# Performance work log

Hardware: AMD Instinct MI355X
Metric: run time of the kernel (lower is better)

Reference implementation:

```python
import jax, jax.numpy as jnp
import numpy as np

EPS = 1e-5


def _ln(t):
    # Custom LayerNorm from the source: unbiased variance (torch.var default),
    # gamma=ones, beta=zeros (plain tensors, never trained) -> plain normalize.
    m = t.mean(axis=-1, keepdims=True)
    v = t.var(axis=-1, keepdims=True, ddof=1)
    return (t - m) / jnp.sqrt(v + EPS)


def setup_inputs() -> dict:
    key = jax.random.key(0)
    B, T, C, H = 4, 2048, 1024, 16
    hs = C // H
    ks = jax.random.split(key, 10)
    s_in = (1.0 / C) ** 0.5   # nn.Linear default init scale (approx, uniform->normal ok for ref)
    s_ff = (1.0 / (4 * C)) ** 0.5
    return {
        "x": jax.random.normal(ks[0], (B, T, C), jnp.float32),
        "Wq": jax.random.normal(ks[1], (H, C, hs), jnp.float32) * s_in,
        "Wk": jax.random.normal(ks[2], (H, C, hs), jnp.float32) * s_in,
        "Wv": jax.random.normal(ks[3], (H, C, hs), jnp.float32) * s_in,
        "Wo": jax.random.normal(ks[4], (C, C), jnp.float32) * s_in,
        "bo": jnp.zeros((C,), jnp.float32),
        "W1": jax.random.normal(ks[5], (C, 4 * C), jnp.float32) * s_in,
        "b1": jnp.zeros((4 * C,), jnp.float32),
        "W2": jax.random.normal(ks[6], (4 * C, C), jnp.float32) * s_ff,
        "b2": jnp.zeros((C,), jnp.float32),
    }


def reference(x, Wq, Wk, Wv, Wo, bo, W1, b1, W2, b2):
    B, T, C = x.shape
    H, _, hs = Wq.shape
    # per-head projections (equivalent to the Python loop over Head modules)
    q = jnp.einsum('btc,hcd->bhtd', x, Wq)
    k = jnp.einsum('btc,hcd->bhtd', x, Wk)
    v = jnp.einsum('btc,hcd->bhtd', x, Wv)
    scores = jnp.einsum('bhtd,bhsd->bhts', q, k) * (hs ** -0.5)
    causal = jnp.tril(jnp.ones((T, T), dtype=bool))
    scores = jnp.where(causal, scores, jnp.float32(-jnp.inf))
    w = jax.nn.softmax(scores, axis=-1)          # dropout is identity in eval
    o = jnp.einsum('bhts,bhsd->bhtd', w, v)
    o = o.transpose(0, 2, 1, 3).reshape(B, T, C)  # concat heads
    attn = o @ Wo + bo
    x1 = x + _ln(attn)
    ff = jax.nn.relu(x1 @ W1 + b1) @ W2 + b2
    return x1 + _ln(ff)
```

## Files before the change

kernel.cpp:

```cpp
#include <hip/hip_runtime.h>
#include <hip/hip_bf16.h>

using bf16 = __hip_bfloat16;
typedef __attribute__((ext_vector_type(8))) short s8v;
typedef __attribute__((ext_vector_type(4))) float f4v;
typedef __attribute__((ext_vector_type(16))) float f16v;
typedef __attribute__((ext_vector_type(4))) unsigned int u4v;

#define QSCALE 0.18033688011112042f

__device__ __forceinline__ void gld_lds16(const void* g, void* l) {
  __builtin_amdgcn_global_load_lds(
      (const __attribute__((address_space(1))) void*)g,
      (__attribute__((address_space(3))) void*)l, 16, 0, 0);
}

__device__ __forceinline__ unsigned short bfbits(float f) {
  bf16 t = __float2bfloat16(f);
  return *reinterpret_cast<unsigned short*>(&t);
}

__device__ __forceinline__ unsigned int pk2(float lo, float hi) {
  return (unsigned int)bfbits(lo) | ((unsigned int)bfbits(hi) << 16);
}

__device__ __forceinline__ void lswap(unsigned int& a, unsigned int& b) {
  asm("v_permlane32_swap_b32 %0, %1" : "+v"(a), "+v"(b));
}

__global__ __launch_bounds__(256) void f32_to_bf16_k(const float* __restrict__ in,
                                                     bf16* __restrict__ out, size_t n) {
  const size_t i = ((size_t)blockIdx.x * 256 + threadIdx.x) * 4;
  if (i + 3 < n) {
    const float4 v = *(const float4*)(in + i);
    out[i + 0] = __float2bfloat16(v.x);
    out[i + 1] = __float2bfloat16(v.y);
    out[i + 2] = __float2bfloat16(v.z);
    out[i + 3] = __float2bfloat16(v.w);
  }
}

__global__ __launch_bounds__(256) void tr_to_bf16_k(const float* __restrict__ in,
                                                    bf16* __restrict__ out,
                                                    int R, int C,
                                                    size_t inb, size_t outb) {
  __shared__ float tile[32][33];
  in  += (size_t)blockIdx.z * inb;
  out += (size_t)blockIdx.z * outb;
  const int r0 = blockIdx.y * 32, c0 = blockIdx.x * 32;
  const int tx = threadIdx.x & 31, ty = threadIdx.x >> 5;
#pragma unroll
  for (int i = 0; i < 4; ++i)
    tile[ty + i * 8][tx] = in[(size_t)(r0 + ty + i * 8) * C + c0 + tx];
  __syncthreads();
#pragma unroll
  for (int i = 0; i < 4; ++i)
    out[(size_t)(c0 + ty + i * 8) * R + r0 + tx] = __float2bfloat16(tile[tx][ty + i * 8]);
}

template <int MODE, int BN>
__global__ __launch_bounds__(512, 2) void gemmT(const bf16* __restrict__ A,
                                                const bf16* __restrict__ B,
                                                const float* __restrict__ bias,
                                                float* __restrict__ Cf,
                                                bf16* __restrict__ Cb,
                                                bf16* __restrict__ Vout,
                                                int M, int N, int K) {
  constexpr int NF = BN / 64;
  constexpr int BH = BN / 128;
  __shared__ __attribute__((aligned(16))) bf16 AS[2][256 * 64];
  __shared__ __attribute__((aligned(16))) bf16 BS[2][BN * 64];

  const int tid  = threadIdx.x;
  const int wid  = tid >> 6;
  const int lane = tid & 63;
  const int l16  = lane & 15;
  const int quad = lane >> 4;
  const int wm   = wid >> 2;
  const int wn   = wid & 3;

  const int gx  = gridDim.x;
  const int nwg = gx * gridDim.y;
  int lin = blockIdx.y * gx + blockIdx.x;
  lin = (lin & 7) * (nwg >> 3) + (lin >> 3);
  const int bm = (lin / gx) * 256;
  const int bn = (lin % gx) * BN;

  const int d0 = tid * 16;
  const int a0 = d0 ^ (((d0 >> 9) & 1) << 5);
  const int sr = a0 >> 7;
  const int scol = (a0 & 127) >> 1;
  const bf16* Asrc = A + (size_t)(bm + sr) * K + scol;
  const bf16* Bsrc = B + (size_t)(bn + sr) * K + scol;
  char* const AW0 = (char*)&AS[0][0] + wid * 1024;
  char* const AW1 = (char*)&AS[1][0] + wid * 1024;
  char* const BW0 = (char*)&BS[0][0] + wid * 1024;
  char* const BW1 = (char*)&BS[1][0] + wid * 1024;

  const int sq16 = (quad * 16) ^ (((l16 >> 2) & 1) << 5);
  const int rdA  = l16 * 128 + sq16;
  const int rdB  = wn * (BN / 4) * 128 + l16 * 128 + sq16;

#define STAGE_A2(dst, src) \
  do { gld_lds16((src), (dst)); gld_lds16((src) + (size_t)64 * K, (dst) + 8192); } while (0)
#define STAGE_BH(dst, src) \
  do { gld_lds16((src), (dst)); \
       if constexpr (BH == 2) gld_lds16((src) + (size_t)64 * K, (dst) + 8192); } while (0)
#define WAIT_B_INFLIGHT() \
  do { if constexpr (BN == 256) asm volatile("s_waitcnt vmcnt(4)" ::: "memory"); \
       else                     asm volatile("s_waitcnt vmcnt(2)" ::: "memory"); } while (0)

  f4v acc[8][NF];
#pragma unroll
  for (int i = 0; i < 8; ++i)
#pragma unroll
    for (int j = 0; j < NF; ++j) acc[i][j] = (f4v){0.f, 0.f, 0.f, 0.f};

  const int NT = K >> 6;

  STAGE_A2(AW0,         Asrc);
  STAGE_A2(AW0 + 16384, Asrc + (size_t)128 * K);
  STAGE_BH(BW0,             Bsrc);
  STAGE_BH(BW0 + BH * 8192, Bsrc + (size_t)(BH * 64) * K);
  STAGE_BH(BW1,             Bsrc + 64);
  STAGE_BH(BW1 + BH * 8192, Bsrc + (size_t)(BH * 64) * K + 64);
  WAIT_B_INFLIGHT();
  asm volatile("s_barrier" ::: "memory");

  s8v bfrag[NF][2];
  for (int u = 0; u < NT; ++u) {
    const int bsel = u & 1;
    const char* Ard = (char*)&AS[bsel][0] + wm * 16384 + rdA;
    const char* Brd = (char*)&BS[bsel][0] + rdB;
    char* const AWn = bsel ? AW0 : AW1;
    char* const BWc = bsel ? BW1 : BW0;
    const bf16* An = Asrc + (size_t)(u + 1) * 64;
    const bf16* Bn = Bsrc + (size_t)(u + 2) * 64;
#pragma unroll
    for (int p = 0; p < 4; ++p) {
      s8v afrag[2][2];
#pragma unroll
      for (int j = 0; j < 2; ++j)
#pragma unroll
        for (int kk = 0; kk < 2; ++kk)
          afrag[j][kk] = *(const s8v*)(Ard + (p * 2 + j) * 2048 + kk * 64);
      if (p == 0) {
#pragma unroll
        for (int nf = 0; nf < NF; ++nf)
#pragma unroll
          for (int kk = 0; kk < 2; ++kk)
            bfrag[nf][kk] = *(const s8v*)(Brd + nf * 2048 + kk * 64);
      }
      if (p == 0 && u + 1 < NT) STAGE_A2(AWn,         An);
      if (p == 1 && u + 1 < NT) STAGE_A2(AWn + 16384, An + (size_t)128 * K);
      if (p == 2 && u + 2 < NT) STAGE_BH(BWc,             Bn);
      if (p == 3 && u + 2 < NT) STAGE_BH(BWc + BH * 8192, Bn + (size_t)(BH * 64) * K);
      asm volatile("s_barrier" ::: "memory");
      asm volatile("s_waitcnt lgkmcnt(0)" ::: "memory");
      __builtin_amdgcn_sched_barrier(0);
      __builtin_amdgcn_s_setprio(1);
#pragma unroll
      for (int kk = 0; kk < 2; ++kk)
#pragma unroll
        for (int j = 0; j < 2; ++j)
#pragma unroll
          for (int nf = 0; nf < NF; ++nf)
            acc[p * 2 + j][nf] = __builtin_amdgcn_mfma_f32_16x16x32_bf16(
                afrag[j][kk], bfrag[nf][kk], acc[p * 2 + j][nf], 0, 0, 0);
      __builtin_amdgcn_s_setprio(0);
      if (p == 3) {
        if (u + 2 < NT) WAIT_B_INFLIGHT();
        else            asm volatile("s_waitcnt vmcnt(0)" ::: "memory");
      }
      asm volatile("s_barrier" ::: "memory");
    }
  }
#undef STAGE_A2
#undef STAGE_BH
#undef WAIT_B_INFLIGHT

  const size_t ldc = (size_t)N;
#pragma unroll
  for (int mf = 0; mf < 8; ++mf) {
#pragma unroll
    for (int nf = 0; nf < NF; ++nf) {
      const int col  = bn + wn * (BN / 4) + nf * 16 + l16;
      const int row0 = bm + wm * 128 + mf * 16 + quad * 4;
      if (MODE == 0) {
        if (col < 2048) {
          const float sc = (col < 1024) ? QSCALE : 1.0f;
#pragma unroll
          for (int r = 0; r < 4; ++r)
            Cb[(size_t)(row0 + r) * ldc + col] = __float2bfloat16(acc[mf][nf][r] * sc);
        } else {
          ushort4 pk;
          pk.x = bfbits(acc[mf][nf][0]);
          pk.y = bfbits(acc[mf][nf][1]);
          pk.z = bfbits(acc[mf][nf][2]);
          pk.w = bfbits(acc[mf][nf][3]);
          const int bb = row0 >> 11, t = row0 & 2047;
          *(ushort4*)&Vout[((size_t)(bb * 1024 + col - 2048)) * 2048 + t] = pk;
        }
      } else {
        const float bv = bias[col];
#pragma unroll
        for (int r = 0; r < 4; ++r) {
          const float v = acc[mf][nf][r] + bv;
          if (MODE == 1) Cf[(size_t)(row0 + r) * ldc + col] = v;
          else           Cb[(size_t)(row0 + r) * ldc + col] = __float2bfloat16(fmaxf(v, 0.f));
        }
      }
    }
  }
}

__global__ __launch_bounds__(256, 3) void attn_mfma(const bf16* __restrict__ qkv,
                                                    const bf16* __restrict__ vtg,
                                                    bf16* __restrict__ o) {
  __shared__ __attribute__((aligned(16))) bf16 KsS[2][64 * 64];
  __shared__ __attribute__((aligned(16))) bf16 VtS[2][64 * 64];
  __shared__ __attribute__((aligned(16))) float tS[128];

  const int tid  = threadIdx.x;
  const int w    = tid >> 6;
  const int lane = tid & 63;
  const int l32  = lane & 31;
  const int hi   = lane >> 5;
  const int xq   = l32 & 7;

  const int lin = blockIdx.x;
  const int b = lin & 3;
  const int h = (lin >> 2) & 15;
  const int qt = 15 - (lin >> 6);

  const bf16* qbase = qkv + (size_t)b * 2048 * 3072 + h * 64;
  const bf16* kbase = qbase + 1024;
  const bf16* vbase = vtg + (size_t)(b * 1024 + h * 64) * 2048;

  const int rsub = lane >> 3;
  const int sseg = (lane & 7) ^ rsub;
  const int d0 = (w * 16) * 64;
  const int d1 = (w * 16 + 8) * 64;

  const int nkt = 2 * qt + 2;
  const int qmin_w = qt * 128 + w * 32;
  const int qmax_w = qmin_w + 31;
  const int q_lane = qmin_w + l32;

  s8v qf[4];
#pragma unroll
  for (int ks = 0; ks < 4; ++ks)
    qf[ks] = *(const s8v*)(qbase + (size_t)q_lane * 3072 + ks * 16 + hi * 8);

  float m_run = -1.0e38f, l_run = 0.f;
  f16v oacc[2];
#pragma unroll
  for (int dn = 0; dn < 2; ++dn)
#pragma unroll
    for (int r = 0; r < 16; ++r) oacc[dn][r] = 0.f;

  const bf16* kg = kbase + (size_t)(w * 16 + rsub) * 3072 + sseg * 8;
  const bf16* vg = vbase + (size_t)(w * 16 + rsub) * 2048 + sseg * 8;

  gld_lds16(kg,                    &KsS[0][d0]);
  gld_lds16(kg + (size_t)8 * 3072, &KsS[0][d1]);
  gld_lds16(vg,                    &VtS[0][d0]);
  gld_lds16(vg + (size_t)8 * 2048, &VtS[0][d1]);
  kg += (size_t)64 * 3072; vg += 64;
  __syncthreads();

  for (int kt = 0; kt < nkt; ++kt) {
    const int cb = kt & 1;

    if (kt + 1 < nkt) {
      const int nb = cb ^ 1;
      gld_lds16(kg,                    &KsS[nb][d0]);
      gld_lds16(kg + (size_t)8 * 3072, &KsS[nb][d1]);
      gld_lds16(vg,                    &VtS[nb][d0]);
      gld_lds16(vg + (size_t)8 * 2048, &VtS[nb][d1]);
      kg += (size_t)64 * 3072; vg += 64;
    }

    if (kt * 64 <= qmax_w) {
      const int kmmax = min(1, (qmax_w - kt * 64) >> 5);
      const bool diag = (kt * 64 + 63 > qmin_w);

      f16v sacc[2];
#pragma unroll
      for (int km = 0; km < 2; ++km)
#pragma unroll
        for (int r = 0; r < 16; ++r) sacc[km][r] = 0.f;

      for (int km = 0; km <= kmmax; ++km)
#pragma unroll
        for (int ks = 0; ks < 4; ++ks) {
          const s8v kf = *(const s8v*)&KsS[cb][(km * 32 + l32) * 64 +
                                               (((2 * ks + hi) ^ xq) << 3)];
          sacc[km] = __builtin_amdgcn_mfma_f32_32x32x16_bf16(kf, qf[ks], sacc[km], 0, 0, 0);
        }

      if (diag) {
        for (int km = 0; km <= kmmax; ++km)
#pragma unroll
          for (int r = 0; r < 16; ++r) {
            const int key = kt * 64 + km * 32 + (r & 3) + 8 * (r >> 2) + 4 * hi;
            if (key > q_lane) sacc[km][r] = -3.0e38f;
          }
      }

      float pmax = -3.0e38f;
#pragma unroll
      for (int km = 0; km < 2; ++km)
        if (km <= kmmax)
#pragma unroll
          for (int r = 0; r < 16; ++r) pmax = fmaxf(pmax, sacc[km][r]);
      pmax = fmaxf(pmax, __shfl_xor(pmax, 32));

      float mref = m_run;
      if (!__all(pmax <= m_run + 8.f)) {
        const float mnew = fmaxf(m_run, pmax);
        const float alpha = __builtin_amdgcn_exp2f(m_run - mnew);
        m_run = mnew; mref = mnew;
        l_run *= alpha;
        tS[w * 32 + l32] = alpha;
        f4v aF[4];
#pragma unroll
        for (int g = 0; g < 4; ++g)
          aF[g] = *(const f4v*)&tS[w * 32 + g * 8 + hi * 4];
#pragma unroll
        for (int dn = 0; dn < 2; ++dn)
#pragma unroll
          for (int r = 0; r < 16; ++r) oacc[dn][r] *= aF[r >> 2][r & 3];
      }

      float rs = 0.f;
      s8v pfr[4];
#pragma unroll
      for (int km = 0; km < 2; ++km)
        if (km <= kmmax) {
          float p[16];
#pragma unroll
          for (int r = 0; r < 16; ++r) {
            p[r] = __builtin_amdgcn_exp2f(sacc[km][r] - mref);
            rs += p[r];
          }
          unsigned int u0 = pk2(p[0], p[1]),  u1 = pk2(p[2], p[3]);
          unsigned int u2 = pk2(p[4], p[5]),  u3 = pk2(p[6], p[7]);
          lswap(u0, u2); lswap(u1, u3);
          u4v f0 = (u4v){u0, u1, u2, u3};
          pfr[2 * km] = *(s8v*)&f0;
          unsigned int v0 = pk2(p[8], p[9]),   v1 = pk2(p[10], p[11]);
          unsigned int v2 = pk2(p[12], p[13]), v3 = pk2(p[14], p[15]);
          lswap(v0, v2); lswap(v1, v3);
          u4v f1 = (u4v){v0, v1, v2, v3};
          pfr[2 * km + 1] = *(s8v*)&f1;
        }
      rs += __shfl_xor(rs, 32);
      l_run += rs;

#pragma unroll
      for (int ks = 0; ks < 4; ++ks)
        if ((ks >> 1) <= kmmax) {
#pragma unroll
          for (int dn = 0; dn < 2; ++dn) {
            const s8v vf = *(const s8v*)&VtS[cb][(dn * 32 + l32) * 64 +
                                                 (((2 * ks + hi) ^ xq) << 3)];
            oacc[dn] = __builtin_amdgcn_mfma_f32_32x32x16_bf16(pfr[ks], vf, oacc[dn], 0, 0, 0);
          }
        }
    }
    __syncthreads();
  }

  tS[w * 32 + l32] = l_run;
  f4v lF[4];
#pragma unroll
  for (int g = 0; g < 4; ++g)
    lF[g] = *(const f4v*)&tS[w * 32 + g * 8 + hi * 4];

#pragma unroll
  for (int r = 0; r < 16; ++r) {
    const float inv = __builtin_amdgcn_rcpf(lF[r >> 2][r & 3]);
    const int row = qt * 128 + w * 32 + (r & 3) + 8 * (r >> 2) + 4 * hi;
    bf16* dst = o + ((size_t)b * 2048 + row) * 1024 + h * 64 + l32;
    dst[0]  = __float2bfloat16(oacc[0][r] * inv);
    dst[32] = __float2bfloat16(oacc[1][r] * inv);
  }
}

__global__ __launch_bounds__(256) void ln_res(const float* __restrict__ xres,
                                              const float* __restrict__ t,
                                              float* __restrict__ xo,
                                              bf16* __restrict__ xob) {
  __shared__ float red[2][4];
  const int tid = threadIdx.x;
  const size_t base = (size_t)blockIdx.x * 1024;
  float v[4];
  float s = 0.f;
#pragma unroll
  for (int i = 0; i < 4; ++i) { v[i] = t[base + tid + i * 256]; s += v[i]; }
#pragma unroll
  for (int off = 32; off > 0; off >>= 1) s += __shfl_xor(s, off, 64);
  if ((tid & 63) == 0) red[0][tid >> 6] = s;
  __syncthreads();
  const float mean = (red[0][0] + red[0][1] + red[0][2] + red[0][3]) * (1.f / 1024.f);
  float ss = 0.f;
#pragma unroll
  for (int i = 0; i < 4; ++i) { const float d = v[i] - mean; ss += d * d; }
#pragma unroll
  for (int off = 32; off > 0; off >>= 1) ss += __shfl_xor(ss, off, 64);
  if ((tid & 63) == 0) red[1][tid >> 6] = ss;
  __syncthreads();
  const float var = (red[1][0] + red[1][1] + red[1][2] + red[1][3]) * (1.f / 1023.f);
  const float rstd = rsqrtf(var + 1e-5f);
#pragma unroll
  for (int i = 0; i < 4; ++i) {
    const size_t idx = base + tid + i * 256;
    const float r = xres[idx] + (v[i] - mean) * rstd;
    xo[idx] = r;
    if (xob) xob[idx] = __float2bfloat16(r);
  }
}

extern "C" void kernel_launch(void* const* d_in, const int* in_sizes, int n_in,
                              void* d_out, int out_size, void* d_ws, size_t ws_size,
                              hipStream_t stream) {
  const float* x  = (const float*)d_in[0];
  const float* Wq = (const float*)d_in[1];
  const float* Wk = (const float*)d_in[2];
  const float* Wv = (const float*)d_in[3];
  const float* Wo = (const float*)d_in[4];
  const float* bo = (const float*)d_in[5];
  const float* W1 = (const float*)d_in[6];
  const float* b1 = (const float*)d_in[7];
  const float* W2 = (const float*)d_in[8];
  const float* b2 = (const float*)d_in[9];
  float* out = (float*)d_out;

  char* ws = (char*)d_ws;
  bf16* qkv_bf = (bf16*)(ws);
  bf16* x_bf   = (bf16*)(ws + 50331648);
  bf16* WqkvT  = (bf16*)(ws + 67108864);
  bf16* WoT    = (bf16*)(ws + 73400320);
  bf16* W1T    = (bf16*)(ws + 75497472);
  bf16* W2T    = (bf16*)(ws + 83886080);
  bf16* o_bf   = (bf16*)(ws + 92274688);
  float* attn  = (float*)(ws + 109051904);
  float* x1    = (float*)(ws + 142606336);
  bf16* x1b    = (bf16*)(ws + 176160768);
  bf16* vt     = (bf16*)(ws + 192937984);
  bf16* h1     = (bf16*)(ws);
  float* ff    = (float*)(ws + 109051904);

  f32_to_bf16_k<<<8192, 256, 0, stream>>>(x, x_bf, (size_t)8388608);
  tr_to_bf16_k<<<dim3(2, 32, 16), 256, 0, stream>>>(Wq, WqkvT,               1024, 64,   65536, 65536);
  tr_to_bf16_k<<<dim3(2, 32, 16), 256, 0, stream>>>(Wk, WqkvT + 1024 * 1024, 1024, 64,   65536, 65536);
  tr_to_bf16_k<<<dim3(2, 32, 16), 256, 0, stream>>>(Wv, WqkvT + 2048 * 1024, 1024, 64,   65536, 65536);
  tr_to_bf16_k<<<dim3(32, 32, 1), 256, 0, stream>>>(Wo, WoT,                 1024, 1024, 0, 0);
  tr_to_bf16_k<<<dim3(128, 32, 1), 256, 0, stream>>>(W1, W1T,                1024, 4096, 0, 0);
  tr_to_bf16_k<<<dim3(32, 128, 1), 256, 0, stream>>>(W2, W2T,                4096, 1024, 0, 0);

  gemmT<0, 256><<<dim3(12, 32), 512, 0, stream>>>(x_bf, WqkvT, nullptr, nullptr, qkv_bf, vt, 8192, 3072, 1024);

  attn_mfma<<<1024, 256, 0, stream>>>(qkv_bf, vt, o_bf);

  gemmT<1, 128><<<dim3(8, 32), 512, 0, stream>>>(o_bf, WoT, bo, attn, nullptr, nullptr, 8192, 1024, 1024);

  ln_res<<<8192, 256, 0, stream>>>(x, attn, x1, x1b);

  gemmT<2, 256><<<dim3(16, 32), 512, 0, stream>>>(x1b, W1T, b1, nullptr, h1, nullptr, 8192, 4096, 1024);

  gemmT<1, 128><<<dim3(8, 32), 512, 0, stream>>>(h1, W2T, b2, ff, nullptr, nullptr, 8192, 1024, 4096);

  ln_res<<<8192, 256, 0, stream>>>(x1, ff, out, nullptr);
}
```

Measured before the change: 509.8 us.

## Pair complementary causal query tiles in one 512-thread attention block

The attention kernel now launches 512-thread blocks where waves 0-3 handle query tile 15-p and waves 4-7 handle tile p of the same batch/head. The two tiles share the K/V tiles staged in LDS, and each block's total work is balanced across the causal triangle. Each thread now issues one K and one V load per tile instead of two, and there are half as many blocks. The cost is larger blocks with more waves held at each __syncthreads, and the waves on the short tile sit idle for the rest of the loop.

```diff
diff --git a/kernel.cpp b/kernel.cpp
--- a/kernel.cpp
+++ b/kernel.cpp
@@ -214,36 +214,41 @@
   }
 }
 
-__global__ __launch_bounds__(256, 3) void attn_mfma(const bf16* __restrict__ qkv,
+__global__ __launch_bounds__(512, 3) void attn_mfma(const bf16* __restrict__ qkv,
                                                     const bf16* __restrict__ vtg,
                                                     bf16* __restrict__ o) {
   __shared__ __attribute__((aligned(16))) bf16 KsS[2][64 * 64];
   __shared__ __attribute__((aligned(16))) bf16 VtS[2][64 * 64];
-  __shared__ __attribute__((aligned(16))) float tS[128];
+  __shared__ __attribute__((aligned(16))) float tS[256];
 
   const int tid  = threadIdx.x;
   const int w    = tid >> 6;
+  const int ww   = w & 3;
   const int lane = tid & 63;
   const int l32  = lane & 31;
   const int hi   = lane >> 5;
   const int xq   = l32 & 7;
 
-  const int lin = blockIdx.x;
-  const int b = lin & 3;
-  const int h = (lin >> 2) & 15;
-  const int qt = 15 - (lin >> 6);
+  const int lin  = blockIdx.x;
+  const int g    = lin & 255;
+  const int half = lin >> 8;
+  const int pidx = g >> 5;
+  const int p    = half ? (7 - pidx) : pidx;
+  const int bh   = (half << 5) | (g & 31);
+  const int b    = bh & 3;
+  const int h    = bh >> 2;
+  const int qt   = (w < 4) ? (15 - p) : p;
 
   const bf16* qbase = qkv + (size_t)b * 2048 * 3072 + h * 64;
   const bf16* kbase = qbase + 1024;
   const bf16* vbase = vtg + (size_t)(b * 1024 + h * 64) * 2048;
 
-  const int rsub = lane >> 3;
-  const int sseg = (lane & 7) ^ rsub;
-  const int d0 = (w * 16) * 64;
-  const int d1 = (w * 16 + 8) * 64;
-
-  const int nkt = 2 * qt + 2;
-  const int qmin_w = qt * 128 + w * 32;
+  const int srow = tid >> 3;
+  const int sseg = (tid & 7) ^ (srow & 7);
+  const int dls  = w * 512;
+
+  const int nkt = 32 - 2 * p;
+  const int qmin_w = qt * 128 + ww * 32;
   const int qmax_w = qmin_w + 31;
   const int q_lane = qmin_w + l32;
 
@@ -259,13 +264,11 @@
 #pragma unroll
     for (int r = 0; r < 16; ++r) oacc[dn][r] = 0.f;
 
-  const bf16* kg = kbase + (size_t)(w * 16 + rsub) * 3072 + sseg * 8;
-  const bf16* vg = vbase + (size_t)(w * 16 + rsub) * 2048 + sseg * 8;
-
-  gld_lds16(kg,                    &KsS[0][d0]);
-  gld_lds16(kg + (size_t)8 * 3072, &KsS[0][d1]);
-  gld_lds16(vg,                    &VtS[0][d0]);
-  gld_lds16(vg + (size_t)8 * 2048, &VtS[0][d1]);
+  const bf16* kg = kbase + (size_t)srow * 3072 + sseg * 8;
+  const bf16* vg = vbase + (size_t)srow * 2048 + sseg * 8;
+
+  gld_lds16(kg, &KsS[0][dls]);
+  gld_lds16(vg, &VtS[0][dls]);
   kg += (size_t)64 * 3072; vg += 64;
   __syncthreads();
 
@@ -274,10 +277,8 @@
 
     if (kt + 1 < nkt) {
       const int nb = cb ^ 1;
-      gld_lds16(kg,                    &KsS[nb][d0]);
-      gld_lds16(kg + (size_t)8 * 3072, &KsS[nb][d1]);
-      gld_lds16(vg,                    &VtS[nb][d0]);
-      gld_lds16(vg + (size_t)8 * 2048, &VtS[nb][d1]);
+      gld_lds16(kg, &KsS[nb][dls]);
+      gld_lds16(vg, &VtS[nb][dls]);
       kg += (size_t)64 * 3072; vg += 64;
     }
 
@@ -325,8 +326,8 @@
         tS[w * 32 + l32] = alpha;
         f4v aF[4];
 #pragma unroll
-        for (int g = 0; g < 4; ++g)
-          aF[g] = *(const f4v*)&tS[w * 32 + g * 8 + hi * 4];
+        for (int g2 = 0; g2 < 4; ++g2)
+          aF[g2] = *(const f4v*)&tS[w * 32 + g2 * 8 + hi * 4];
 #pragma unroll
         for (int dn = 0; dn < 2; ++dn)
 #pragma unroll
@@ -338,19 +339,19 @@
 #pragma unroll
       for (int km = 0; km < 2; ++km)
         if (km <= kmmax) {
-          float p[16];
+          float pv[16];
 #pragma unroll
           for (int r = 0; r < 16; ++r) {
-            p[r] = __builtin_amdgcn_exp2f(sacc[km][r] - mref);
-            rs += p[r];
+            pv[r] = __builtin_amdgcn_exp2f(sacc[km][r] - mref);
+            rs += pv[r];
           }
-          unsigned int u0 = pk2(p[0], p[1]),  u1 = pk2(p[2], p[3]);
-          unsigned int u2 = pk2(p[4], p[5]),  u3 = pk2(p[6], p[7]);
+          unsigned int u0 = pk2(pv[0], pv[1]),  u1 = pk2(pv[2], pv[3]);
+          unsigned int u2 = pk2(pv[4], pv[5]),  u3 = pk2(pv[6], pv[7]);
           lswap(u0, u2); lswap(u1, u3);
           u4v f0 = (u4v){u0, u1, u2, u3};
           pfr[2 * km] = *(s8v*)&f0;
-          unsigned int v0 = pk2(p[8], p[9]),   v1 = pk2(p[10], p[11]);
-          unsigned int v2 = pk2(p[12], p[13]), v3 = pk2(p[14], p[15]);
+          unsigned int v0 = pk2(pv[8], pv[9]),   v1 = pk2(pv[10], pv[11]);
+          unsigned int v2 = pk2(pv[12], pv[13]), v3 = pk2(pv[14], pv[15]);
           lswap(v0, v2); lswap(v1, v3);
           u4v f1 = (u4v){v0, v1, v2, v3};
           pfr[2 * km + 1] = *(s8v*)&f1;
@@ -375,13 +376,13 @@
   tS[w * 32 + l32] = l_run;
   f4v lF[4];
 #pragma unroll
-  for (int g = 0; g < 4; ++g)
-    lF[g] = *(const f4v*)&tS[w * 32 + g * 8 + hi * 4];
+  for (int g2 = 0; g2 < 4; ++g2)
+    lF[g2] = *(const f4v*)&tS[w * 32 + g2 * 8 + hi * 4];
 
 #pragma unroll
   for (int r = 0; r < 16; ++r) {
     const float inv = __builtin_amdgcn_rcpf(lF[r >> 2][r & 3]);
-    const int row = qt * 128 + w * 32 + (r & 3) + 8 * (r >> 2) + 4 * hi;
+    const int row = qt * 128 + ww * 32 + (r & 3) + 8 * (r >> 2) + 4 * hi;
     bf16* dst = o + ((size_t)b * 2048 + row) * 1024 + h * 64 + l32;
     dst[0]  = __float2bfloat16(oacc[0][r] * inv);
     dst[32] = __float2bfloat16(oacc[1][r] * inv);
@@ -462,7 +463,7 @@
 
   gemmT<0, 256><<<dim3(12, 32), 512, 0, stream>>>(x_bf, WqkvT, nullptr, nullptr, qkv_bf, vt, 8192, 3072, 1024);
 
-  attn_mfma<<<1024, 256, 0, stream>>>(qkv_bf, vt, o_bf);
+  attn_mfma<<<512, 512, 0, stream>>>(qkv_bf, vt, o_bf);
 
   gemmT<1, 128><<<dim3(8, 32), 512, 0, stream>>>(o_bf, WoT, bo, attn, nullptr, nullptr, 8192, 1024, 1024);
 
```

New measurement: 550.1 us. 7.9% more time.

## Pair light and heavy causal query tiles per block and use explicit waitcnt barriers

Applied to the files above, without the earlier changes.

Each attention block now handles two query tiles, p and 15-p, one after the other, so every block does the same amount of causal work and the grid halves to 512 blocks. The per-iteration __syncthreads is replaced with manual s_waitcnt vmcnt plus s_barrier, so the block waits only for the current K/V tile's async LDS loads while the next tile's prefetch stays in flight. This targets load imbalance and the tail effect from uneven causal tiles. In exchange there are fewer blocks to hide latency, and the hand-written waitcnt depends on the compiler emitting no other outstanding vector memory operations.

```diff
diff --git a/kernel.cpp b/kernel.cpp
--- a/kernel.cpp
+++ b/kernel.cpp
@@ -231,7 +231,7 @@
   const int lin = blockIdx.x;
   const int b = lin & 3;
   const int h = (lin >> 2) & 15;
-  const int qt = 15 - (lin >> 6);
+  const int p = lin >> 6;
 
   const bf16* qbase = qkv + (size_t)b * 2048 * 3072 + h * 64;
   const bf16* kbase = qbase + 1024;
@@ -242,149 +242,155 @@
   const int d0 = (w * 16) * 64;
   const int d1 = (w * 16 + 8) * 64;
 
-  const int nkt = 2 * qt + 2;
-  const int qmin_w = qt * 128 + w * 32;
-  const int qmax_w = qmin_w + 31;
-  const int q_lane = qmin_w + l32;
-
-  s8v qf[4];
-#pragma unroll
-  for (int ks = 0; ks < 4; ++ks)
-    qf[ks] = *(const s8v*)(qbase + (size_t)q_lane * 3072 + ks * 16 + hi * 8);
-
-  float m_run = -1.0e38f, l_run = 0.f;
-  f16v oacc[2];
-#pragma unroll
-  for (int dn = 0; dn < 2; ++dn)
-#pragma unroll
-    for (int r = 0; r < 16; ++r) oacc[dn][r] = 0.f;
-
-  const bf16* kg = kbase + (size_t)(w * 16 + rsub) * 3072 + sseg * 8;
-  const bf16* vg = vbase + (size_t)(w * 16 + rsub) * 2048 + sseg * 8;
-
-  gld_lds16(kg,                    &KsS[0][d0]);
-  gld_lds16(kg + (size_t)8 * 3072, &KsS[0][d1]);
-  gld_lds16(vg,                    &VtS[0][d0]);
-  gld_lds16(vg + (size_t)8 * 2048, &VtS[0][d1]);
-  kg += (size_t)64 * 3072; vg += 64;
-  __syncthreads();
-
-  for (int kt = 0; kt < nkt; ++kt) {
-    const int cb = kt & 1;
-
-    if (kt + 1 < nkt) {
-      const int nb = cb ^ 1;
-      gld_lds16(kg,                    &KsS[nb][d0]);
-      gld_lds16(kg + (size_t)8 * 3072, &KsS[nb][d1]);
-      gld_lds16(vg,                    &VtS[nb][d0]);
-      gld_lds16(vg + (size_t)8 * 2048, &VtS[nb][d1]);
-      kg += (size_t)64 * 3072; vg += 64;
-    }
-
-    if (kt * 64 <= qmax_w) {
-      const int kmmax = min(1, (qmax_w - kt * 64) >> 5);
-      const bool diag = (kt * 64 + 63 > qmin_w);
-
-      f16v sacc[2];
-#pragma unroll
-      for (int km = 0; km < 2; ++km)
-#pragma unroll
-        for (int r = 0; r < 16; ++r) sacc[km][r] = 0.f;
-
-      for (int km = 0; km <= kmmax; ++km)
-#pragma unroll
-        for (int ks = 0; ks < 4; ++ks) {
-          const s8v kf = *(const s8v*)&KsS[cb][(km * 32 + l32) * 64 +
-                                               (((2 * ks + hi) ^ xq) << 3)];
-          sacc[km] = __builtin_amdgcn_mfma_f32_32x32x16_bf16(kf, qf[ks], sacc[km], 0, 0, 0);
+  for (int phase = 0; phase < 2; ++phase) {
+    const int qt  = phase ? (15 - p) : p;
+    const int nkt = 2 * qt + 2;
+    const int qmin_w = qt * 128 + w * 32;
+    const int qmax_w = qmin_w + 31;
+    const int q_lane = qmin_w + l32;
+
+    s8v qf[4];
+#pragma unroll
+    for (int ks = 0; ks < 4; ++ks)
+      qf[ks] = *(const s8v*)(qbase + (size_t)q_lane * 3072 + ks * 16 + hi * 8);
+
+    float m_run = -1.0e38f, l_run = 0.f;
+    f16v oacc[2];
+#pragma unroll
+    for (int dn = 0; dn < 2; ++dn)
+#pragma unroll
+      for (int r = 0; r < 16; ++r) oacc[dn][r] = 0.f;
+
+    const bf16* kg = kbase + (size_t)(w * 16 + rsub) * 3072 + sseg * 8;
+    const bf16* vg = vbase + (size_t)(w * 16 + rsub) * 2048 + sseg * 8;
+
+    gld_lds16(kg,                    &KsS[0][d0]);
+    gld_lds16(kg + (size_t)8 * 3072, &KsS[0][d1]);
+    gld_lds16(vg,                    &VtS[0][d0]);
+    gld_lds16(vg + (size_t)8 * 2048, &VtS[0][d1]);
+    kg += (size_t)64 * 3072; vg += 64;
+
+    for (int kt = 0; kt < nkt; ++kt) {
+      const int cb = kt & 1;
+
+      if (kt + 1 < nkt) {
+        const int nb = cb ^ 1;
+        gld_lds16(kg,                    &KsS[nb][d0]);
+        gld_lds16(kg + (size_t)8 * 3072, &KsS[nb][d1]);
+        gld_lds16(vg,                    &VtS[nb][d0]);
+        gld_lds16(vg + (size_t)8 * 2048, &VtS[nb][d1]);
+        kg += (size_t)64 * 3072; vg += 64;
+        asm volatile("s_waitcnt vmcnt(4)" ::: "memory");
+      } else {
+        asm volatile("s_waitcnt vmcnt(0)" ::: "memory");
+      }
+      asm volatile("s_barrier" ::: "memory");
+
+      if (kt * 64 <= qmax_w) {
+        const int kmmax = min(1, (qmax_w - kt * 64) >> 5);
+        const bool diag = (kt * 64 + 63 > qmin_w);
+
+        f16v sacc[2];
+#pragma unroll
+        for (int km = 0; km < 2; ++km)
+#pragma unroll
+          for (int r = 0; r < 16; ++r) sacc[km][r] = 0.f;
+
+        for (int km = 0; km <= kmmax; ++km)
+#pragma unroll
+          for (int ks = 0; ks < 4; ++ks) {
+            const s8v kf = *(const s8v*)&KsS[cb][(km * 32 + l32) * 64 +
+                                                 (((2 * ks + hi) ^ xq) << 3)];
+            sacc[km] = __builtin_amdgcn_mfma_f32_32x32x16_bf16(kf, qf[ks], sacc[km], 0, 0, 0);
+          }
+
+        if (diag) {
+          for (int km = 0; km <= kmmax; ++km)
+#pragma unroll
+            for (int r = 0; r < 16; ++r) {
+              const int key = kt * 64 + km * 32 + (r & 3) + 8 * (r >> 2) + 4 * hi;
+              if (key > q_lane) sacc[km][r] = -3.0e38f;
+            }
         }
 
-      if (diag) {
-        for (int km = 0; km <= kmmax; ++km)
-#pragma unroll
-          for (int r = 0; r < 16; ++r) {
-            const int key = kt * 64 + km * 32 + (r & 3) + 8 * (r >> 2) + 4 * hi;
-            if (key > q_lane) sacc[km][r] = -3.0e38f;
+        float pmax = -3.0e38f;
+#pragma unroll
+        for (int km = 0; km < 2; ++km)
+          if (km <= kmmax)
+#pragma unroll
+            for (int r = 0; r < 16; ++r) pmax = fmaxf(pmax, sacc[km][r]);
+        pmax = fmaxf(pmax, __shfl_xor(pmax, 32));
+
+        float mref = m_run;
+        if (!__all(pmax <= m_run + 8.f)) {
+          const float mnew = fmaxf(m_run, pmax);
+          const float alpha = __builtin_amdgcn_exp2f(m_run - mnew);
+          m_run = mnew; mref = mnew;
+          l_run *= alpha;
+          tS[w * 32 + l32] = alpha;
+          f4v aF[4];
+#pragma unroll
+          for (int g2 = 0; g2 < 4; ++g2)
+            aF[g2] = *(const f4v*)&tS[w * 32 + g2 * 8 + hi * 4];
+#pragma unroll
+          for (int dn = 0; dn < 2; ++dn)
+#pragma unroll
+            for (int r = 0; r < 16; ++r) oacc[dn][r] *= aF[r >> 2][r & 3];
+        }
+
+        float rs = 0.f;
+        s8v pfr[4];
+#pragma unroll
+        for (int km = 0; km < 2; ++km)
+          if (km <= kmmax) {
+            float pv[16];
+#pragma unroll
+            for (int r = 0; r < 16; ++r) {
+              pv[r] = __builtin_amdgcn_exp2f(sacc[km][r] - mref);
+              rs += pv[r];
+            }
+            unsigned int u0 = pk2(pv[0], pv[1]),  u1 = pk2(pv[2], pv[3]);
+            unsigned int u2 = pk2(pv[4], pv[5]),  u3 = pk2(pv[6], pv[7]);
+            lswap(u0, u2); lswap(u1, u3);
+            u4v f0 = (u4v){u0, u1, u2, u3};
+            pfr[2 * km] = *(s8v*)&f0;
+            unsigned int v0 = pk2(pv[8], pv[9]),   v1 = pk2(pv[10], pv[11]);
+            unsigned int v2 = pk2(pv[12], pv[13]), v3 = pk2(pv[14], pv[15]);
+            lswap(v0, v2); lswap(v1, v3);
+            u4v f1 = (u4v){v0, v1, v2, v3};
+            pfr[2 * km + 1] = *(s8v*)&f1;
+          }
+        rs += __shfl_xor(rs, 32);
+        l_run += rs;
+
+#pragma unroll
+        for (int ks = 0; ks < 4; ++ks)
+          if ((ks >> 1) <= kmmax) {
+#pragma unroll
+            for (int dn = 0; dn < 2; ++dn) {
+              const s8v vf = *(const s8v*)&VtS[cb][(dn * 32 + l32) * 64 +
+                                                   (((2 * ks + hi) ^ xq) << 3)];
+              oacc[dn] = __builtin_amdgcn_mfma_f32_32x32x16_bf16(pfr[ks], vf, oacc[dn], 0, 0, 0);
+            }
           }
       }
-
-      float pmax = -3.0e38f;
-#pragma unroll
-      for (int km = 0; km < 2; ++km)
-        if (km <= kmmax)
-#pragma unroll
-          for (int r = 0; r < 16; ++r) pmax = fmaxf(pmax, sacc[km][r]);
-      pmax = fmaxf(pmax, __shfl_xor(pmax, 32));
-
-      float mref = m_run;
-      if (!__all(pmax <= m_run + 8.f)) {
-        const float mnew = fmaxf(m_run, pmax);
-        const float alpha = __builtin_amdgcn_exp2f(m_run - mnew);
-        m_run = mnew; mref = mnew;
-        l_run *= alpha;
-        tS[w * 32 + l32] = alpha;
-        f4v aF[4];
-#pragma unroll
-        for (int g = 0; g < 4; ++g)
-          aF[g] = *(const f4v*)&tS[w * 32 + g * 8 + hi * 4];
-#pragma unroll
-        for (int dn = 0; dn < 2; ++dn)
-#pragma unroll
-          for (int r = 0; r < 16; ++r) oacc[dn][r] *= aF[r >> 2][r & 3];
-      }
-
-      float rs = 0.f;
-      s8v pfr[4];
-#pragma unroll
-      for (int km = 0; km < 2; ++km)
-        if (km <= kmmax) {
-          float p[16];
-#pragma unroll
-          for (int r = 0; r < 16; ++r) {
-            p[r] = __builtin_amdgcn_exp2f(sacc[km][r] - mref);
-            rs += p[r];
-          }
-          unsigned int u0 = pk2(p[0], p[1]),  u1 = pk2(p[2], p[3]);
-          unsigned int u2 = pk2(p[4], p[5]),  u3 = pk2(p[6], p[7]);
-          lswap(u0, u2); lswap(u1, u3);
-          u4v f0 = (u4v){u0, u1, u2, u3};
-          pfr[2 * km] = *(s8v*)&f0;
-          unsigned int v0 = pk2(p[8], p[9]),   v1 = pk2(p[10], p[11]);
-          unsigned int v2 = pk2(p[12], p[13]), v3 = pk2(p[14], p[15]);
-          lswap(v0, v2); lswap(v1, v3);
-          u4v f1 = (u4v){v0, v1, v2, v3};
-          pfr[2 * km + 1] = *(s8v*)&f1;
-        }
-      rs += __shfl_xor(rs, 32);
-      l_run += rs;
-
-#pragma unroll
-      for (int ks = 0; ks < 4; ++ks)
-        if ((ks >> 1) <= kmmax) {
-#pragma unroll
-          for (int dn = 0; dn < 2; ++dn) {
-            const s8v vf = *(const s8v*)&VtS[cb][(dn * 32 + l32) * 64 +
-                                                 (((2 * ks + hi) ^ xq) << 3)];
-            oacc[dn] = __builtin_amdgcn_mfma_f32_32x32x16_bf16(pfr[ks], vf, oacc[dn], 0, 0, 0);
-          }
-        }
+      asm volatile("s_barrier" ::: "memory");
     }
-    __syncthreads();
-  }
-
-  tS[w * 32 + l32] = l_run;
-  f4v lF[4];
-#pragma unroll
-  for (int g = 0; g < 4; ++g)
-    lF[g] = *(const f4v*)&tS[w * 32 + g * 8 + hi * 4];
-
-#pragma unroll
-  for (int r = 0; r < 16; ++r) {
-    const float inv = __builtin_amdgcn_rcpf(lF[r >> 2][r & 3]);
-    const int row = qt * 128 + w * 32 + (r & 3) + 8 * (r >> 2) + 4 * hi;
-    bf16* dst = o + ((size_t)b * 2048 + row) * 1024 + h * 64 + l32;
-    dst[0]  = __float2bfloat16(oacc[0][r] * inv);
-    dst[32] = __float2bfloat16(oacc[1][r] * inv);
+
+    tS[w * 32 + l32] = l_run;
+    f4v lF[4];
+#pragma unroll
+    for (int g2 = 0; g2 < 4; ++g2)
+      lF[g2] = *(const f4v*)&tS[w * 32 + g2 * 8 + hi * 4];
+
+#pragma unroll
+    for (int r = 0; r < 16; ++r) {
+      const float inv = __builtin_amdgcn_rcpf(lF[r >> 2][r & 3]);
+      const int row = qt * 128 + w * 32 + (r & 3) + 8 * (r >> 2) + 4 * hi;
+      bf16* dst = o + ((size_t)b * 2048 + row) * 1024 + h * 64 + l32;
+      dst[0]  = __float2bfloat16(oacc[0][r] * inv);
+      dst[32] = __float2bfloat16(oacc[1][r] * inv);
+    }
   }
 }
 
@@ -462,7 +468,7 @@
 
   gemmT<0, 256><<<dim3(12, 32), 512, 0, stream>>>(x_bf, WqkvT, nullptr, nullptr, qkv_bf, vt, 8192, 3072, 1024);
 
-  attn_mfma<<<1024, 256, 0, stream>>>(qkv_bf, vt, o_bf);
+  attn_mfma<<<512, 256, 0, stream>>>(qkv_bf, vt, o_bf);
 
   gemmT<1, 128><<<dim3(8, 32), 512, 0, stream>>>(o_bf, WoT, bo, attn, nullptr, nullptr, 8192, 1024, 1024);
 
```

After: 528.9 us. 3.7% more time.
